# Performance work log

Hardware: AMD Instinct MI355X
Metric: run time of the kernel (lower is better)

Reference implementation:

```python
import jax, jax.numpy as jnp
import numpy as np

POOLING_RATIO = 0.5  # matches init kwarg
N_NODES = 16384
N_EDGES = 524288
D_FEAT = 128


def setup_inputs() -> dict:
    key = jax.random.key(0)
    k1, k2, k3, k4 = jax.random.split(key, 4)
    return {
        "pos": jax.random.normal(k1, (N_NODES, 3), jnp.float32),
        "feat": jax.random.normal(k2, (N_NODES, D_FEAT), jnp.float32),
        "src": jax.random.randint(k3, (N_EDGES,), 0, N_NODES, jnp.int32),
        "dst": jax.random.randint(k4, (N_EDGES,), 0, N_NODES, jnp.int32),
        "batch_size": 4,
    }


def _fps(p, k):
    # Farthest point sampling on one cloud p: [n, 3]. Deterministic start at idx 0
    # (DGL uses a random start; we fix it for reproducibility).
    n = p.shape[0]
    def step(carry, _):
        dists, last = carry  # dists: min sq-dist to selected set so far
        d = jnp.sum((p - p[last]) ** 2, axis=-1)
        dists = jnp.minimum(dists, d)
        nxt = jnp.argmax(dists).astype(jnp.int32)
        return (dists, nxt), last
    init = (jnp.full((n,), 1e10, p.dtype), jnp.asarray(0, jnp.int32))
    _, idx = jax.lax.scan(step, init, None, length=k)
    return idx  # [k]


def reference(pos, feat, src, dst, batch_size):
    N = pos.shape[0]
    n_points = N // batch_size
    k = round(n_points * (1.0 - POOLING_RATIO))  # downsampled points per cloud

    # ---- farthest point sampling per cloud ----
    p = pos.reshape(batch_size, n_points, pos.shape[-1])  # [B, n, 3]
    fp = jax.vmap(lambda q: _fps(q, k))(p)                # [B, k] local ids
    offs = (jnp.arange(batch_size, dtype=jnp.int32) * n_points)[:, None]
    fp_idx = (fp + offs).reshape(-1)                      # [B*k] global ids

    # ---- copy_u + mean aggregation on the FULL graph (G.update_all) ----
    deg = jax.ops.segment_sum(jnp.ones_like(dst, dtype=feat.dtype), dst, num_segments=N)
    agg = jax.ops.segment_sum(feat[src], dst, num_segments=N)  # [N, D]
    agg = agg / jnp.maximum(deg, 1.0)[:, None]  # nodes with no in-edges stay 0

    # ---- induced subgraph gather ----
    M = fp_idx.shape[0]
    sub_x = pos[fp_idx]      # [M, 3]
    sub_feat = agg[fp_idx]   # [M, D]

    # induced subgraph edges: keep original edges whose endpoints are both sampled
    inv = jnp.full((N,), -1, jnp.int32).at[fp_idx].set(jnp.arange(M, dtype=jnp.int32))
    ls, ld = inv[src], inv[dst]
    edge_mask = (ls >= 0) & (ld >= 0)
    ls = jnp.where(edge_mask, ls, 0)
    ld = jnp.where(edge_mask, ld, 0)

    # per-edge displacement and norm on subgraph positions
    d = jnp.where(edge_mask[:, None], sub_x[ld] - sub_x[ls], 0.0)  # [E, 3]
    w = jnp.sqrt(jnp.sum(d ** 2, axis=-1, keepdims=True))          # [E, 1]

    return sub_x, sub_feat, d, w, edge_mask, fp_idx
```

## Files before the change

kernel.cpp:

```cpp
#include <hip/hip_runtime.h>
#include <math.h>

#define N_NODES 16384
#define N_EDGES 524288
#define D_FEAT  128
#define BATCH   4
#define NPTS    4096
#define KSEL    2048
#define MSEL    (BATCH*KSEL)

typedef float f32x2 __attribute__((ext_vector_type(2)));

#define PK_ADD(D,A,B) asm("v_pk_add_f32 %0, %1, %2" : "=v"(D) : "v"(A), "v"(B))
#define PK_MUL(D,A,B) asm("v_pk_mul_f32 %0, %1, %2" : "=v"(D) : "v"(A), "v"(B))

#define X8(F) F(0) F(1) F(2) F(3) F(4) F(5) F(6) F(7)

template <int CTRL>
__device__ __forceinline__ unsigned long long dpp_u64(unsigned long long p)
{
    unsigned slo = (unsigned)__builtin_amdgcn_update_dpp(
        0, (int)(unsigned)p, CTRL, 0xf, 0xf, true);
    unsigned shi = (unsigned)__builtin_amdgcn_update_dpp(
        0, (int)(unsigned)(p >> 32), CTRL, 0xf, 0xf, true);
    return (((unsigned long long)shi) << 32) | slo;
}
__device__ __forceinline__ unsigned long long max_u64(unsigned long long a,
                                                      unsigned long long b)
{
    return (b > a) ? b : a;
}

__launch_bounds__(256, 1)
__global__ void fps_deg_kernel(const float* __restrict__ pos,
                               int* __restrict__ fp_int,
                               int* __restrict__ inv,
                               float* __restrict__ out_subx,
                               float* __restrict__ out_fp,
                               const int* __restrict__ dst,
                               int* __restrict__ deg)
{
    __shared__ float sx[NPTS];
    __shared__ float sy[NPTS];
    __shared__ float sz[NPTS];
    __shared__ int   sel[KSEL];
    __shared__ unsigned long long pwv[2][4];

    if (blockIdx.x >= BATCH) {
        int e = (blockIdx.x - BATCH) * 256 + threadIdx.x;
        atomicAdd(&deg[dst[e]], 1);
        return;
    }

    const int b    = blockIdx.x;
    const int tid  = threadIdx.x;
    const int lane = tid & 63;
    const int wv   = tid >> 6;

    const float* gp = pos + (size_t)b * NPTS * 3;
    for (int i = tid; i < NPTS; i += 256) {
        sx[i] = gp[3 * i + 0];
        sy[i] = gp[3 * i + 1];
        sz[i] = gp[3 * i + 2];
    }
    __syncthreads();

#define DECL(M) f32x2 x##M, y##M, z##M, d##M;
    X8(DECL)
#undef DECL
#define LOAD(M) { \
        int l0 = (2*(M))*256 + tid, l1 = (2*(M)+1)*256 + tid; \
        x##M.x = sx[l0]; x##M.y = sx[l1]; \
        y##M.x = sy[l0]; y##M.y = sy[l1]; \
        z##M.x = sz[l0]; z##M.y = sz[l1]; \
        d##M.x = 1e10f;  d##M.y = 1e10f; }
    X8(LOAD)
#undef LOAD

    float qx = sx[0], qy = sy[0], qz = sz[0];
    int cur = 0;

    for (int t = 0; t < KSEL; ++t) {
        if (tid == 0) sel[t] = cur;

        f32x2 nqx, nqy, nqz;
        nqx.x = -qx; nqx.y = -qx;
        nqy.x = -qy; nqy.y = -qy;
        nqz.x = -qz; nqz.y = -qz;

        float bv = -1.0f;
        int   bj = 0;
#define UPD2(M) { \
        f32x2 dx, dy, dz, mx, my, mz, s1, dd; \
        PK_ADD(dx, x##M, nqx); PK_ADD(dy, y##M, nqy); PK_ADD(dz, z##M, nqz); \
        PK_MUL(mx, dx, dx); PK_MUL(my, dy, dy); PK_MUL(mz, dz, dz); \
        PK_ADD(s1, mx, my); PK_ADD(dd, s1, mz); \
        float n0 = fminf(d##M.x, dd.x); d##M.x = n0; \
        if (n0 > bv) { bv = n0; bj = 2*(M); } \
        float n1 = fminf(d##M.y, dd.y); d##M.y = n1; \
        if (n1 > bv) { bv = n1; bj = 2*(M)+1; } }
        X8(UPD2)
#undef UPD2

        int bi = (bj << 8) + tid;

        unsigned long long p =
            (((unsigned long long)__float_as_uint(bv)) << 32) |
            (unsigned)(~bi);

        p = max_u64(p, dpp_u64<0x111>(p));
        p = max_u64(p, dpp_u64<0x112>(p));
        p = max_u64(p, dpp_u64<0x114>(p));
        p = max_u64(p, dpp_u64<0x118>(p));
        p = max_u64(p, dpp_u64<0x142>(p));
        p = max_u64(p, dpp_u64<0x143>(p));

        int par = t & 1;
        if (lane == 63) pwv[par][wv] = p;
        __syncthreads();

        unsigned long long c0 = pwv[par][0];
        unsigned long long c1 = pwv[par][1];
        unsigned long long c2 = pwv[par][2];
        unsigned long long c3 = pwv[par][3];
        unsigned long long m01 = (c1 > c0) ? c1 : c0;
        unsigned long long m23 = (c3 > c2) ? c3 : c2;
        unsigned long long mm  = (m23 > m01) ? m23 : m01;
        cur = (int)(~(unsigned)(mm & 0xffffffffULL));

        qx = sx[cur]; qy = sy[cur]; qz = sz[cur];
    }
    __syncthreads();

    for (int t = tid; t < KSEL; t += 256) {
        int c = sel[t];
        int g = b * NPTS + c;
        int m = b * KSEL + t;
        fp_int[m] = g;
        inv[g] = m;
        out_fp[m] = (float)g;
        out_subx[m * 3 + 0] = sx[c];
        out_subx[m * 3 + 1] = sy[c];
        out_subx[m * 3 + 2] = sz[c];
    }
}

__global__ void scan_kernel(const int* __restrict__ deg, int* __restrict__ row_ptr)
{
    __shared__ int part[1024];
    int tid = threadIdx.x;
    int base = tid * 16;
    int local[16];
    int s = 0;
#pragma unroll
    for (int j = 0; j < 16; ++j) { local[j] = s; s += deg[base + j]; }
    part[tid] = s;
    __syncthreads();
    for (int off = 1; off < 1024; off <<= 1) {
        int v = part[tid];
        int add = (tid >= off) ? part[tid - off] : 0;
        __syncthreads();
        part[tid] = v + add;
        __syncthreads();
    }
    int prefix = (tid == 0) ? 0 : part[tid - 1];
#pragma unroll
    for (int j = 0; j < 16; ++j) row_ptr[base + j] = prefix + local[j];
    if (tid == 1023) row_ptr[N_NODES] = part[1023];
}

__global__ void scatter_kernel(const int* __restrict__ src, const int* __restrict__ dst,
                               const int* __restrict__ row_ptr, int* __restrict__ cursor,
                               int* __restrict__ col)
{
    int e = blockIdx.x * blockDim.x + threadIdx.x;
    if (e < N_EDGES) {
        int d0 = dst[e];
        int r = atomicAdd(&cursor[d0], 1);
        col[row_ptr[d0] + r] = src[e];
    }
}

__global__ void agg_edge_kernel(const float* __restrict__ feat,
                                const int* __restrict__ fp_int,
                                const int* __restrict__ row_ptr,
                                const int* __restrict__ col,
                                const int* __restrict__ deg,
                                float* __restrict__ out_subfeat,
                                const int* __restrict__ src,
                                const int* __restrict__ dst,
                                const int* __restrict__ inv,
                                const float* __restrict__ subx,
                                float* __restrict__ outd,
                                float* __restrict__ outw,
                                float* __restrict__ outm)
{
    if (blockIdx.x < 2048) {
        int wid  = (blockIdx.x * blockDim.x + threadIdx.x) >> 6;
        int lane = threadIdx.x & 63;
        int v  = fp_int[wid];
        int s0 = row_ptr[v];
        int s1 = row_ptr[v + 1];
        float a0 = 0.0f, a1 = 0.0f;
        for (int e = s0; e < s1; ++e) {
            int s = col[e];
            const float2* f2 = (const float2*)(feat + (size_t)s * D_FEAT);
            float2 vv = f2[lane];
            a0 += vv.x;
            a1 += vv.y;
        }
        float dv = fmaxf((float)deg[v], 1.0f);
        float* o = out_subfeat + (size_t)wid * D_FEAT + lane * 2;
        o[0] = a0 / dv;
        o[1] = a1 / dv;
    } else {
        int e = (blockIdx.x - 2048) * blockDim.x + threadIdx.x;
        int ls = inv[src[e]];
        int ld = inv[dst[e]];
        bool mk = (ls >= 0) && (ld >= 0);
        float dx = 0.0f, dy = 0.0f, dz = 0.0f;
        if (mk) {
            dx = __fsub_rn(subx[ld * 3 + 0], subx[ls * 3 + 0]);
            dy = __fsub_rn(subx[ld * 3 + 1], subx[ls * 3 + 1]);
            dz = __fsub_rn(subx[ld * 3 + 2], subx[ls * 3 + 2]);
        }
        float w = sqrtf(__fadd_rn(__fadd_rn(__fmul_rn(dx, dx), __fmul_rn(dy, dy)),
                                  __fmul_rn(dz, dz)));
        outd[e * 3 + 0] = dx;
        outd[e * 3 + 1] = dy;
        outd[e * 3 + 2] = dz;
        outw[e] = w;
        outm[e] = mk ? 1.0f : 0.0f;
    }
}

extern "C" void kernel_launch(void* const* d_in, const int* in_sizes, int n_in,
                              void* d_out, int out_size, void* d_ws, size_t ws_size,
                              hipStream_t stream)
{
    const float* pos  = (const float*)d_in[0];
    const float* feat = (const float*)d_in[1];
    const int*   src  = (const int*)d_in[2];
    const int*   dst  = (const int*)d_in[3];

    float* out = (float*)d_out;
    float* out_subx    = out;
    float* out_subfeat = out_subx + (size_t)MSEL * 3;
    float* out_d       = out_subfeat + (size_t)MSEL * D_FEAT;
    float* out_w       = out_d + (size_t)N_EDGES * 3;
    float* out_m       = out_w + (size_t)N_EDGES;
    float* out_fp      = out_m + (size_t)N_EDGES;

    int* fp_int  = (int*)d_ws;
    int* inv     = fp_int + MSEL;
    int* deg     = inv + N_NODES;
    int* row_ptr = deg + N_NODES;
    int* cursor  = row_ptr + (N_NODES+1);
    int* col     = cursor + N_NODES;

    (void)hipMemsetAsync(inv,    0xFF, (size_t)N_NODES * 4, stream);
    (void)hipMemsetAsync(deg,    0,    (size_t)N_NODES * 4, stream);
    (void)hipMemsetAsync(cursor, 0,    (size_t)N_NODES * 4, stream);

    fps_deg_kernel<<<BATCH + N_EDGES / 256, 256, 0, stream>>>(
        pos, fp_int, inv, out_subx, out_fp, dst, deg);

    scan_kernel<<<1, 1024, 0, stream>>>(deg, row_ptr);
    scatter_kernel<<<N_EDGES / 256, 256, 0, stream>>>(src, dst, row_ptr, cursor, col);

    agg_edge_kernel<<<4096, 256, 0, stream>>>(feat, fp_int, row_ptr, col, deg,
                                              out_subfeat, src, dst, inv, out_subx,
                                              out_d, out_w, out_m);
}
```

Before: 1.339 ms.

## Split degree counting from FPS, pack positions as float4, tree-reduce per-thread argmax

After: 1.398 ms. +4.4%, slower.

```diff
diff --git a/kernel.cpp b/kernel.cpp
--- a/kernel.cpp
+++ b/kernel.cpp
@@ -32,25 +32,15 @@
 }
 
 __launch_bounds__(256, 1)
-__global__ void fps_deg_kernel(const float* __restrict__ pos,
-                               int* __restrict__ fp_int,
-                               int* __restrict__ inv,
-                               float* __restrict__ out_subx,
-                               float* __restrict__ out_fp,
-                               const int* __restrict__ dst,
-                               int* __restrict__ deg)
-{
-    __shared__ float sx[NPTS];
-    __shared__ float sy[NPTS];
-    __shared__ float sz[NPTS];
-    __shared__ int   sel[KSEL];
+__global__ void fps_kernel(const float* __restrict__ pos,
+                           int* __restrict__ fp_int,
+                           int* __restrict__ inv,
+                           float* __restrict__ out_subx,
+                           float* __restrict__ out_fp)
+{
+    __shared__ float4 s4[NPTS];
+    __shared__ int    sel[KSEL];
     __shared__ unsigned long long pwv[2][4];
-
-    if (blockIdx.x >= BATCH) {
-        int e = (blockIdx.x - BATCH) * 256 + threadIdx.x;
-        atomicAdd(&deg[dst[e]], 1);
-        return;
-    }
 
     const int b    = blockIdx.x;
     const int tid  = threadIdx.x;
@@ -59,9 +49,7 @@
 
     const float* gp = pos + (size_t)b * NPTS * 3;
     for (int i = tid; i < NPTS; i += 256) {
-        sx[i] = gp[3 * i + 0];
-        sy[i] = gp[3 * i + 1];
-        sz[i] = gp[3 * i + 2];
+        s4[i] = make_float4(gp[3 * i + 0], gp[3 * i + 1], gp[3 * i + 2], 0.0f);
     }
     __syncthreads();
 
@@ -69,15 +57,16 @@
     X8(DECL)
 #undef DECL
 #define LOAD(M) { \
-        int l0 = (2*(M))*256 + tid, l1 = (2*(M)+1)*256 + tid; \
-        x##M.x = sx[l0]; x##M.y = sx[l1]; \
-        y##M.x = sy[l0]; y##M.y = sy[l1]; \
-        z##M.x = sz[l0]; z##M.y = sz[l1]; \
-        d##M.x = 1e10f;  d##M.y = 1e10f; }
+        float4 a = s4[(2*(M))*256 + tid]; \
+        float4 c = s4[(2*(M)+1)*256 + tid]; \
+        x##M.x = a.x; x##M.y = c.x; \
+        y##M.x = a.y; y##M.y = c.y; \
+        z##M.x = a.z; z##M.y = c.z; \
+        d##M.x = 1e10f; d##M.y = 1e10f; }
     X8(LOAD)
 #undef LOAD
 
-    float qx = sx[0], qy = sy[0], qz = sz[0];
+    float qx = s4[0].x, qy = s4[0].y, qz = s4[0].z;
     int cur = 0;
 
     for (int t = 0; t < KSEL; ++t) {
@@ -88,20 +77,27 @@
         nqy.x = -qy; nqy.y = -qy;
         nqz.x = -qz; nqz.y = -qz;
 
-        float bv = -1.0f;
-        int   bj = 0;
+        float pv0,pv1,pv2,pv3,pv4,pv5,pv6,pv7;
+        int   pj0,pj1,pj2,pj3,pj4,pj5,pj6,pj7;
 #define UPD2(M) { \
         f32x2 dx, dy, dz, mx, my, mz, s1, dd; \
         PK_ADD(dx, x##M, nqx); PK_ADD(dy, y##M, nqy); PK_ADD(dz, z##M, nqz); \
         PK_MUL(mx, dx, dx); PK_MUL(my, dy, dy); PK_MUL(mz, dz, dz); \
         PK_ADD(s1, mx, my); PK_ADD(dd, s1, mz); \
         float n0 = fminf(d##M.x, dd.x); d##M.x = n0; \
-        if (n0 > bv) { bv = n0; bj = 2*(M); } \
         float n1 = fminf(d##M.y, dd.y); d##M.y = n1; \
-        if (n1 > bv) { bv = n1; bj = 2*(M)+1; } }
+        pv##M = (n1 > n0) ? n1 : n0; \
+        pj##M = (n1 > n0) ? (2*(M)+1) : (2*(M)); }
         X8(UPD2)
 #undef UPD2
 
+#define NODE(VA, JA, VB, JB, VO, JO) \
+        float VO = (VB > VA) ? VB : VA; int JO = (VB > VA) ? JB : JA;
+        NODE(pv0, pj0, pv1, pj1, tA, jA)  NODE(pv2, pj2, pv3, pj3, tB, jB)
+        NODE(pv4, pj4, pv5, pj5, tC, jC)  NODE(pv6, pj6, pv7, pj7, tD, jD)
+        NODE(tA, jA, tB, jB, tE, jE)      NODE(tC, jC, tD, jD, tF, jF)
+        NODE(tE, jE, tF, jF, bv, bj)
+#undef NODE
         int bi = (bj << 8) + tid;
 
         unsigned long long p =
@@ -128,21 +124,29 @@
         unsigned long long mm  = (m23 > m01) ? m23 : m01;
         cur = (int)(~(unsigned)(mm & 0xffffffffULL));
 
-        qx = sx[cur]; qy = sy[cur]; qz = sz[cur];
+        float4 q = s4[cur];
+        qx = q.x; qy = q.y; qz = q.z;
     }
     __syncthreads();
 
     for (int t = tid; t < KSEL; t += 256) {
         int c = sel[t];
+        float4 q = s4[c];
         int g = b * NPTS + c;
         int m = b * KSEL + t;
         fp_int[m] = g;
         inv[g] = m;
         out_fp[m] = (float)g;
-        out_subx[m * 3 + 0] = sx[c];
-        out_subx[m * 3 + 1] = sy[c];
-        out_subx[m * 3 + 2] = sz[c];
-    }
+        out_subx[m * 3 + 0] = q.x;
+        out_subx[m * 3 + 1] = q.y;
+        out_subx[m * 3 + 2] = q.z;
+    }
+}
+
+__global__ void deg_kernel(const int* __restrict__ dst, int* __restrict__ deg)
+{
+    int e = blockIdx.x * blockDim.x + threadIdx.x;
+    if (e < N_EDGES) atomicAdd(&deg[dst[e]], 1);
 }
 
 __global__ void scan_kernel(const int* __restrict__ deg, int* __restrict__ row_ptr)
@@ -262,11 +266,11 @@
     (void)hipMemsetAsync(deg,    0,    (size_t)N_NODES * 4, stream);
     (void)hipMemsetAsync(cursor, 0,    (size_t)N_NODES * 4, stream);
 
-    fps_deg_kernel<<<BATCH + N_EDGES / 256, 256, 0, stream>>>(
-        pos, fp_int, inv, out_subx, out_fp, dst, deg);
-
+    deg_kernel<<<N_EDGES / 256, 256, 0, stream>>>(dst, deg);
     scan_kernel<<<1, 1024, 0, stream>>>(deg, row_ptr);
     scatter_kernel<<<N_EDGES / 256, 256, 0, stream>>>(src, dst, row_ptr, cursor, col);
+
+    fps_kernel<<<BATCH, 256, 0, stream>>>(pos, fp_int, inv, out_subx, out_fp);
 
     agg_edge_kernel<<<4096, 256, 0, stream>>>(feat, fp_int, row_ptr, col, deg,
                                               out_subfeat, src, dst, inv, out_subx,
```
